# Optimization experiments

Measured on AMD Instinct MI355X. Metric: run time of the kernel, lower is better.

## Reference

```python
import jax, jax.numpy as jnp
import numpy as np

N_NODES = 100000
N_EDGES = 1600000
D_FEAT = 128
ALPHA = 0.1
K_STEPS = 10


def setup_inputs() -> dict:
    key = jax.random.key(0)
    k1, k2, k3 = jax.random.split(key, 3)
    x = jax.random.normal(k1, (N_NODES, D_FEAT), dtype=jnp.float32)
    edge_index = jax.random.randint(k2, (2, N_EDGES), 0, N_NODES, dtype=jnp.int64)
    edge_vals = jax.random.uniform(k3, (N_EDGES,), dtype=jnp.float32)
    return {"x": x, "edge_index": edge_index, "edge_vals": edge_vals}


def _spmm(edge_index, edge_vals, h, n_nodes):
    # out[i] = sum_j A[i, j] * h[j]; row = edge_index[0], col = edge_index[1]
    row, col = edge_index[0], edge_index[1]
    msgs = edge_vals[:, None] * h[col]  # [E, d]
    return jax.ops.segment_sum(msgs, row, num_segments=n_nodes)


def reference(x, edge_index, edge_vals):
    # APPNP propagation: h <- (1 - alpha) * A @ h + alpha * x, K steps.
    # dropout=0.0 -> dropout is the identity (as in the torch module default).
    def body(_, h):
        return (1.0 - ALPHA) * _spmm(edge_index, edge_vals, h, N_NODES) + ALPHA * x

    return jax.lax.fori_loop(0, K_STEPS, body, x)
```

## Files before the change

kernel.cpp:

```cpp
#include <hip/hip_runtime.h>


#define N_NODES 100000
#define N_EDGES 1600000
#define D_FEAT  128
#define ALPHA   0.1f
#define K_STEPS 10
#define MAXDEG  64

#define NBUCK 196
#define BCAP  16000
#define EPB_A 2048

#define SCAN_ELEMS 512
#define SCAN_NBLK  ((N_NODES + SCAN_ELEMS - 1) / SCAN_ELEMS)

static __device__ __forceinline__ float bf2f(unsigned u16) {
    return __uint_as_float(u16 << 16);
}
static __device__ __forceinline__ unsigned f2bf(float f) {
    unsigned u = __float_as_uint(f);
    return (u + 0x7fffu + ((u >> 16) & 1u)) >> 16;
}


__global__ __launch_bounds__(256) void bucket_scatter(const int* __restrict__ rows,
                                                      const int* __restrict__ cols,
                                                      const float* __restrict__ w,
                                                      int* __restrict__ gcount,
                                                      int4* __restrict__ gbuf) {
    __shared__ int h_cnt[NBUCK];
    __shared__ int h_base[NBUCK];
    __shared__ int h_cur[NBUCK];
    const int tid = threadIdx.x;
    for (int i = tid; i < NBUCK; i += 256) { h_cnt[i] = 0; h_cur[i] = 0; }
    __syncthreads();

    const int base_e = blockIdx.x * EPB_A + tid;
    int er[8]; int ec[8]; float ew[8];
    #pragma unroll
    for (int k = 0; k < 8; ++k) {
        int e = base_e + k * 256;
        bool v = (e < N_EDGES);
        er[k] = v ? rows[e] : -1;
        ec[k] = v ? cols[e] : 0;
        ew[k] = v ? w[e] : 0.f;
        if (v) atomicAdd(&h_cnt[er[k] >> 9], 1);
    }
    __syncthreads();
    for (int i = tid; i < NBUCK; i += 256) {
        h_base[i] = (h_cnt[i] > 0) ? atomicAdd(&gcount[i], h_cnt[i]) : 0;
    }
    __syncthreads();
    #pragma unroll
    for (int k = 0; k < 8; ++k) {
        if (er[k] >= 0) {
            int b = er[k] >> 9;
            int p = h_base[b] + atomicAdd(&h_cur[b], 1);
            if (p < BCAP) {
                int4 ent;
                ent.x = er[k];
                ent.y = ec[k];
                ent.z = __float_as_int((1.0f - ALPHA) * ew[k]);
                ent.w = 0;
                gbuf[(size_t)b * BCAP + p] = ent;
            }
        }
    }
}

__global__ __launch_bounds__(256) void bucket_to_csr(const int* __restrict__ gcount,
                                                     const int4* __restrict__ gbuf,
                                                     int* __restrict__ cnt,
                                                     int2* __restrict__ csrp) {
    __shared__ int rcur[512];
    const int tid = threadIdx.x;
    const int b = blockIdx.x;
    for (int i = tid; i < 512; i += 256) rcur[i] = 0;
    __syncthreads();
    int n = gcount[b];
    if (n > BCAP) n = BCAP;
    for (int i = tid; i < n; i += 256) {
        int4 e = gbuf[(size_t)b * BCAP + i];
        int p = atomicAdd(&rcur[e.x & 511], 1);
        if (p < MAXDEG) {
            int2 cw;
            cw.x = e.y;
            cw.y = e.z;
            csrp[((size_t)e.x << 6) + p] = cw;
        }
    }
    __syncthreads();
    const int rowbase = b << 9;
    for (int i = tid; i < 512; i += 256) {
        int row = rowbase + i;
        if (row < N_NODES) cnt[row] = rcur[i];
    }
}


__global__ __launch_bounds__(256) void hist_kernel(const int* __restrict__ rows,
                                                   int* __restrict__ deg) {
    int e = blockIdx.x * 256 + threadIdx.x;
    if (e < N_EDGES) atomicAdd(&deg[rows[e]], 1);
}

__global__ __launch_bounds__(256) void scan_partial(const int* __restrict__ deg,
                                                    int* __restrict__ partial) {
    __shared__ int s[256];
    int b = blockIdx.x, t = threadIdx.x;
    int i0 = b * SCAN_ELEMS + t * 2;
    int v0 = (i0 < N_NODES) ? deg[i0] : 0;
    int v1 = (i0 + 1 < N_NODES) ? deg[i0 + 1] : 0;
    s[t] = v0 + v1;
    __syncthreads();
    for (int off = 128; off > 0; off >>= 1) {
        if (t < off) s[t] += s[t + off];
        __syncthreads();
    }
    if (t == 0) partial[b] = s[0];
}

__global__ __launch_bounds__(256) void scan_top(int* __restrict__ partial) {
    __shared__ int s[256];
    int t = threadIdx.x;
    s[t] = (t < SCAN_NBLK) ? partial[t] : 0;
    __syncthreads();
    for (int off = 1; off < 256; off <<= 1) {
        int v = (t >= off) ? s[t - off] : 0;
        __syncthreads();
        s[t] += v;
        __syncthreads();
    }
    if (t < SCAN_NBLK) partial[t] = (t == 0) ? 0 : s[t - 1];
}

__global__ __launch_bounds__(256) void scan_final(int* __restrict__ deg_cursor,
                                                  const int* __restrict__ partial,
                                                  int* __restrict__ row_ptr) {
    __shared__ int s[256];
    int b = blockIdx.x, t = threadIdx.x;
    int i0 = b * SCAN_ELEMS + t * 2;
    int v0 = (i0 < N_NODES) ? deg_cursor[i0] : 0;
    int v1 = (i0 + 1 < N_NODES) ? deg_cursor[i0 + 1] : 0;
    int pair = v0 + v1;
    s[t] = pair;
    __syncthreads();
    for (int off = 1; off < 256; off <<= 1) {
        int v = (t >= off) ? s[t - off] : 0;
        __syncthreads();
        s[t] += v;
        __syncthreads();
    }
    int ex = partial[b] + s[t] - pair;
    if (i0 < N_NODES)     { row_ptr[i0] = ex;          deg_cursor[i0] = ex; }
    if (i0 + 1 < N_NODES) { row_ptr[i0 + 1] = ex + v0; deg_cursor[i0 + 1] = ex + v0; }
    if (b == 0 && t == 0) row_ptr[N_NODES] = N_EDGES;
}

__global__ __launch_bounds__(256) void scatter_kernel(const int* __restrict__ rows,
                                                      const int* __restrict__ cols,
                                                      const float* __restrict__ w,
                                                      int* __restrict__ cursor,
                                                      int2* __restrict__ csr) {
    int e = blockIdx.x * 256 + threadIdx.x;
    if (e < N_EDGES) {
        int pos = atomicAdd(&cursor[rows[e]], 1);
        int2 cw;
        cw.x = cols[e];
        cw.y = __float_as_int((1.0f - ALPHA) * w[e]);
        csr[pos] = cw;
    }
}

__global__ __launch_bounds__(256) void x_to_bf16(const float2* __restrict__ x2,
                                                 unsigned* __restrict__ xb, int n) {
    int i = blockIdx.x * 256 + threadIdx.x;
    if (i < n) {
        float2 v = x2[i];
        xb[i] = f2bf(v.x) | (f2bf(v.y) << 16);
    }
}


template <bool SRC_BF, bool DST_BF, bool X_BF, bool PAD>
__global__ __launch_bounds__(256) void row_spmm_t(const int* __restrict__ rp,
                                                  const int2* __restrict__ csr,
                                                  const void* __restrict__ xsrc,
                                                  const void* __restrict__ src,
                                                  void* __restrict__ dst) {
    int row = (blockIdx.x * 256 + threadIdx.x) >> 6;
    int lane = threadIdx.x & 63;
    if (row >= N_NODES) return;
    int beg, end;
    if (PAD) {
        int cn = rp[row];
        cn = (cn < MAXDEG) ? cn : MAXDEG;
        beg = row << 6;
        end = beg + cn;
    } else {
        beg = rp[row];
        end = rp[row + 1];
    }

    float xtx, xty;
    if (X_BF) {
        unsigned u = ((const unsigned*)xsrc)[(size_t)row * 64 + lane];
        xtx = ALPHA * bf2f(u & 0xffffu);
        xty = ALPHA * bf2f(u >> 16);
    } else {
        float2 xv = ((const float2*)xsrc)[(size_t)row * 64 + lane];
        xtx = ALPHA * xv.x;
        xty = ALPHA * xv.y;
    }

    const float2*   sf = (const float2*)src;
    const unsigned* sb = (const unsigned*)src;

    float ax[4] = {0.f, 0.f, 0.f, 0.f};
    float ay[4] = {0.f, 0.f, 0.f, 0.f};

    auto gather = [&](int col) -> float2 {
        if (SRC_BF) {
            unsigned u = sb[(size_t)col * 64 + lane];
            float2 v;
            v.x = bf2f(u & 0xffffu);
            v.y = bf2f(u >> 16);
            return v;
        } else {
            return sf[(size_t)col * 64 + lane];
        }
    };

    int j = beg;
    while (j + 16 <= end) {
        int2 cw[16];
        #pragma unroll
        for (int u = 0; u < 16; ++u) cw[u] = csr[j + u];
        float2 v[16];
        #pragma unroll
        for (int u = 0; u < 16; ++u) v[u] = gather(cw[u].x);
        #pragma unroll
        for (int u = 0; u < 16; ++u) {
            float wv = __int_as_float(cw[u].y);
            ax[u & 3] += wv * v[u].x;
            ay[u & 3] += wv * v[u].y;
        }
        j += 16;
    }
    while (j + 8 <= end) {
        int2 cw[8];
        #pragma unroll
        for (int u = 0; u < 8; ++u) cw[u] = csr[j + u];
        float2 v[8];
        #pragma unroll
        for (int u = 0; u < 8; ++u) v[u] = gather(cw[u].x);
        #pragma unroll
        for (int u = 0; u < 8; ++u) {
            float wv = __int_as_float(cw[u].y);
            ax[u & 3] += wv * v[u].x;
            ay[u & 3] += wv * v[u].y;
        }
        j += 8;
    }
    while (j + 4 <= end) {
        int2 cw[4];
        #pragma unroll
        for (int u = 0; u < 4; ++u) cw[u] = csr[j + u];
        float2 v[4];
        #pragma unroll
        for (int u = 0; u < 4; ++u) v[u] = gather(cw[u].x);
        #pragma unroll
        for (int u = 0; u < 4; ++u) {
            float wv = __int_as_float(cw[u].y);
            ax[u] += wv * v[u].x;
            ay[u] += wv * v[u].y;
        }
        j += 4;
    }
    for (; j < end; ++j) {
        int2 cw = csr[j];
        float2 v = gather(cw.x);
        float wv = __int_as_float(cw.y);
        ax[0] += wv * v.x;
        ay[0] += wv * v.y;
    }

    float ox = xtx + (ax[0] + ax[1]) + (ax[2] + ax[3]);
    float oy = xty + (ay[0] + ay[1]) + (ay[2] + ay[3]);

    if (DST_BF) {
        ((unsigned*)dst)[(size_t)row * 64 + lane] = f2bf(ox) | (f2bf(oy) << 16);
    } else {
        float2 o; o.x = ox; o.y = oy;
        ((float2*)dst)[(size_t)row * 64 + lane] = o;
    }
}


__global__ __launch_bounds__(256) void init_step(const float4* __restrict__ x,
                                                 float4* __restrict__ dst, int n4) {
    int i = blockIdx.x * 256 + threadIdx.x;
    if (i < n4) {
        float4 v = x[i];
        dst[i] = make_float4(ALPHA * v.x, ALPHA * v.y, ALPHA * v.z, ALPHA * v.w);
    }
}

__global__ __launch_bounds__(256) void edge_scatter(const int* __restrict__ rows,
                                                    const int* __restrict__ cols,
                                                    const float* __restrict__ w,
                                                    const float* __restrict__ h,
                                                    float* __restrict__ dst) {
    unsigned t = blockIdx.x * 256u + threadIdx.x;
    unsigned e = t >> 5;
    unsigned l = t & 31u;
    if (e >= N_EDGES) return;
    int r = rows[e];
    int c = cols[e];
    float we = (1.0f - ALPHA) * w[e];
    const float4* hc = (const float4*)(h + (size_t)c * D_FEAT);
    float4 v = hc[l];
    float* dr = dst + (size_t)r * D_FEAT + (size_t)l * 4;
    unsafeAtomicAdd(dr + 0, we * v.x);
    unsafeAtomicAdd(dr + 1, we * v.y);
    unsafeAtomicAdd(dr + 2, we * v.z);
    unsafeAtomicAdd(dr + 3, we * v.w);
}

extern "C" void kernel_launch(void* const* d_in, const int* in_sizes, int n_in,
                              void* d_out, int out_size, void* d_ws, size_t ws_size,
                              hipStream_t stream) {
    const float* x  = (const float*)d_in[0];
    const int*   ei = (const int*)d_in[1];
    const float* ev = (const float*)d_in[2];
    const int* rows = ei;
    const int* cols = ei + N_EDGES;
    float* out = (float*)d_out;

    auto align512 = [](size_t o) { return (o + 511) & ~(size_t)511; };

    size_t p_off = 0;
    size_t p_ha   = p_off; p_off = align512(p_off + (size_t)N_NODES * D_FEAT * 2);
    size_t p_hb   = p_off; p_off = align512(p_off + (size_t)N_NODES * D_FEAT * 2);
    size_t p_xb   = p_off; p_off = align512(p_off + (size_t)N_NODES * D_FEAT * 2);
    size_t p_cnt  = p_off; p_off = align512(p_off + (size_t)N_NODES * 4 + NBUCK * 4);
    size_t p_csr  = p_off; p_off = align512(p_off + (size_t)N_NODES * MAXDEG * 8);
    size_t need_pad = p_off;
    static_assert((size_t)NBUCK * BCAP * 16 <= 2 * (size_t)N_NODES * D_FEAT * 2,
                  "gbuf must fit in hb+xb");

    size_t c_off = 0;
    size_t c_ha      = c_off; c_off = align512(c_off + (size_t)N_NODES * D_FEAT * 2);
    size_t c_hb      = c_off; c_off = align512(c_off + (size_t)N_NODES * D_FEAT * 2);
    size_t c_rowptr  = c_off; c_off = align512(c_off + (size_t)(N_NODES + 1) * 4);
    size_t c_cursor  = c_off; c_off = align512(c_off + (size_t)N_NODES * 4);
    size_t c_partial = c_off; c_off = align512(c_off + (size_t)SCAN_NBLK * 4);
    size_t c_csr     = c_off; c_off = align512(c_off + (size_t)N_EDGES * 8);
    size_t need_base = c_off;
    size_t c_xb      = c_off; c_off = align512(c_off + (size_t)N_NODES * D_FEAT * 2);
    size_t need_xb   = c_off;

    const int row_blocks = (N_NODES * 64 + 255) / 256;
    const float2* x2 = (const float2*)x;

    if (ws_size >= need_pad) {
        char* ws = (char*)d_ws;
        void*     h_a    = (void*)(ws + p_ha);
        void*     h_b    = (void*)(ws + p_hb);
        unsigned* xb     = (unsigned*)(ws + p_xb);
        int*      cnt    = (int*)(ws + p_cnt);
        int*      gcount = cnt + N_NODES;
        int2*     csrp   = (int2*)(ws + p_csr);
        int4*     gbuf   = (int4*)(ws + p_hb);

        hipMemsetAsync(cnt, 0, (size_t)N_NODES * 4 + NBUCK * 4, stream);
        const int blocks_a = (N_EDGES + EPB_A - 1) / EPB_A;
        bucket_scatter<<<blocks_a, 256, 0, stream>>>(rows, cols, ev, gcount, gbuf);
        bucket_to_csr<<<NBUCK, 256, 0, stream>>>(gcount, gbuf, cnt, csrp);

        const int nxb = N_NODES * D_FEAT / 2;
        x_to_bf16<<<(nxb + 255) / 256, 256, 0, stream>>>(x2, xb, nxb);

        row_spmm_t<true, true, true, true><<<row_blocks, 256, 0, stream>>>(
            cnt, csrp, (const void*)xb, (const void*)xb, h_a);
        for (int k = 1; k <= 8; ++k) {
            const void* src = (k & 1) ? h_a : h_b;
            void* dst = (k & 1) ? h_b : h_a;
            row_spmm_t<true, true, true, true><<<row_blocks, 256, 0, stream>>>(
                cnt, csrp, (const void*)xb, src, dst);
        }
        row_spmm_t<true, false, false, true><<<row_blocks, 256, 0, stream>>>(
            cnt, csrp, (const void*)x2, (const void*)h_a, (void*)out);
    } else if (ws_size >= need_base) {
        char* ws = (char*)d_ws;
        void*  h_a     = (void*)(ws + c_ha);
        void*  h_b     = (void*)(ws + c_hb);
        int*   row_ptr = (int*)(ws + c_rowptr);
        int*   cursor  = (int*)(ws + c_cursor);
        int*   partial = (int*)(ws + c_partial);
        int2*  csr     = (int2*)(ws + c_csr);
        unsigned* xb   = (unsigned*)(ws + c_xb);
        const bool has_xb = (ws_size >= need_xb);
        const int edge_blocks_1t = (N_EDGES + 255) / 256;

        hipMemsetAsync(cursor, 0, (size_t)N_NODES * 4, stream);
        hist_kernel<<<edge_blocks_1t, 256, 0, stream>>>(rows, cursor);
        scan_partial<<<SCAN_NBLK, 256, 0, stream>>>(cursor, partial);
        scan_top<<<1, 256, 0, stream>>>(partial);
        scan_final<<<SCAN_NBLK, 256, 0, stream>>>(cursor, partial, row_ptr);
        scatter_kernel<<<edge_blocks_1t, 256, 0, stream>>>(rows, cols, ev, cursor, csr);

        if (has_xb) {
            const int nxb = N_NODES * D_FEAT / 2;
            x_to_bf16<<<(nxb + 255) / 256, 256, 0, stream>>>(x2, xb, nxb);
            row_spmm_t<true, true, true, false><<<row_blocks, 256, 0, stream>>>(
                row_ptr, csr, (const void*)xb, (const void*)xb, h_a);
            for (int k = 1; k <= 8; ++k) {
                const void* src = (k & 1) ? h_a : h_b;
                void* dst = (k & 1) ? h_b : h_a;
                row_spmm_t<true, true, true, false><<<row_blocks, 256, 0, stream>>>(
                    row_ptr, csr, (const void*)xb, src, dst);
            }
            row_spmm_t<true, false, false, false><<<row_blocks, 256, 0, stream>>>(
                row_ptr, csr, (const void*)x2, (const void*)h_a, (void*)out);
        } else {
            row_spmm_t<false, true, false, false><<<row_blocks, 256, 0, stream>>>(
                row_ptr, csr, (const void*)x2, (const void*)x, h_a);
            for (int k = 1; k <= 8; ++k) {
                const void* src = (k & 1) ? h_a : h_b;
                void* dst = (k & 1) ? h_b : h_a;
                row_spmm_t<true, true, false, false><<<row_blocks, 256, 0, stream>>>(
                    row_ptr, csr, (const void*)x2, src, dst);
            }
            row_spmm_t<true, false, false, false><<<row_blocks, 256, 0, stream>>>(
                row_ptr, csr, (const void*)x2, (const void*)h_a, (void*)out);
        }
    } else {
        float* wsf = (float*)d_ws;
        const int n4 = N_NODES * D_FEAT / 4;
        const int init_blocks = (n4 + 255) / 256;
        const int edge_blocks = (N_EDGES * 32 + 255) / 256;
        for (int k = 0; k < K_STEPS; ++k) {
            const float* src = (k == 0) ? x : ((k & 1) ? wsf : out);
            float* dst = (k & 1) ? out : wsf;
            init_step<<<init_blocks, 256, 0, stream>>>((const float4*)x, (float4*)dst, n4);
            edge_scatter<<<edge_blocks, 256, 0, stream>>>(rows, cols, ev, src, dst);
        }
    }
}
```

Measured before the change: 804.3 us.

## Split each row's wavefront into four edge groups with 16-byte bf16 gathers

Adds a new SpMM kernel in which each 64-lane wavefront handles one row as four 16-lane subgroups. Each subgroup processes different edges and gathers a full 256-byte bf16 feature row with uint4 loads, and the partial sums are combined with cross-lane shuffles. This replaces narrow 4-byte-per-lane gathers and serial per-edge iteration with wider loads and more edges in flight, aiming for better memory-level parallelism on a gather-bound kernel. The CSR buffer is padded by 512 bytes so the out-of-range index reads stay in bounds. The 16-edge unroll in the old kernel, now used only on the fallback path, is removed.

```diff
diff --git a/kernel.cpp b/kernel.cpp
--- a/kernel.cpp
+++ b/kernel.cpp
@@ -179,6 +179,110 @@
     if (i < n) {
         float2 v = x2[i];
         xb[i] = f2bf(v.x) | (f2bf(v.y) << 16);
+    }
+}
+
+
+template <bool DST_BF, bool X_BF>
+__global__ __launch_bounds__(256) void row_spmm_q(const int* __restrict__ rp,
+                                                  const int2* __restrict__ csr,
+                                                  const void* __restrict__ xsrc,
+                                                  const unsigned* __restrict__ src,
+                                                  void* __restrict__ dst) {
+    int row = (blockIdx.x * 256 + threadIdx.x) >> 6;
+    int lane = threadIdx.x & 63;
+    if (row >= N_NODES) return;
+    int cn = rp[row];
+    cn = (cn < MAXDEG) ? cn : MAXDEG;
+    const int beg = row << 6;
+    const int end = beg + cn;
+    const int sub = lane >> 4;
+    const int fl  = lane & 15;
+
+    uint4 xu; float4 xa, xc;
+    if (X_BF) {
+        xu = ((const uint4*)xsrc)[(size_t)row * 16 + fl];
+    } else {
+        xa = ((const float4*)xsrc)[(size_t)row * 32 + 2 * fl];
+        xc = ((const float4*)xsrc)[(size_t)row * 32 + 2 * fl + 1];
+    }
+
+    const uint4* s4 = (const uint4*)src;
+
+    float acc[8];
+    #pragma unroll
+    for (int k = 0; k < 8; ++k) acc[k] = 0.f;
+
+    for (int j = beg; j < end; j += 8) {
+        int i0 = j + sub;
+        int i1 = j + 4 + sub;
+        bool v0 = i0 < end;
+        bool v1 = i1 < end;
+        int2 c0 = csr[i0];
+        int2 c1 = csr[i1];
+        int col0 = v0 ? c0.x : 0;
+        int col1 = v1 ? c1.x : 0;
+        float w0 = v0 ? __int_as_float(c0.y) : 0.f;
+        float w1 = v1 ? __int_as_float(c1.y) : 0.f;
+        uint4 g0 = s4[(size_t)col0 * 16 + fl];
+        uint4 g1 = s4[(size_t)col1 * 16 + fl];
+        acc[0] += w0 * bf2f(g0.x & 0xffffu);
+        acc[1] += w0 * bf2f(g0.x >> 16);
+        acc[2] += w0 * bf2f(g0.y & 0xffffu);
+        acc[3] += w0 * bf2f(g0.y >> 16);
+        acc[4] += w0 * bf2f(g0.z & 0xffffu);
+        acc[5] += w0 * bf2f(g0.z >> 16);
+        acc[6] += w0 * bf2f(g0.w & 0xffffu);
+        acc[7] += w0 * bf2f(g0.w >> 16);
+        acc[0] += w1 * bf2f(g1.x & 0xffffu);
+        acc[1] += w1 * bf2f(g1.x >> 16);
+        acc[2] += w1 * bf2f(g1.y & 0xffffu);
+        acc[3] += w1 * bf2f(g1.y >> 16);
+        acc[4] += w1 * bf2f(g1.z & 0xffffu);
+        acc[5] += w1 * bf2f(g1.z >> 16);
+        acc[6] += w1 * bf2f(g1.w & 0xffffu);
+        acc[7] += w1 * bf2f(g1.w >> 16);
+    }
+
+    #pragma unroll
+    for (int k = 0; k < 8; ++k) {
+        acc[k] += __shfl_xor(acc[k], 16);
+        acc[k] += __shfl_xor(acc[k], 32);
+    }
+
+    if (X_BF) {
+        acc[0] += ALPHA * bf2f(xu.x & 0xffffu);
+        acc[1] += ALPHA * bf2f(xu.x >> 16);
+        acc[2] += ALPHA * bf2f(xu.y & 0xffffu);
+        acc[3] += ALPHA * bf2f(xu.y >> 16);
+        acc[4] += ALPHA * bf2f(xu.z & 0xffffu);
+        acc[5] += ALPHA * bf2f(xu.z >> 16);
+        acc[6] += ALPHA * bf2f(xu.w & 0xffffu);
+        acc[7] += ALPHA * bf2f(xu.w >> 16);
+    } else {
+        acc[0] += ALPHA * xa.x; acc[1] += ALPHA * xa.y;
+        acc[2] += ALPHA * xa.z; acc[3] += ALPHA * xa.w;
+        acc[4] += ALPHA * xc.x; acc[5] += ALPHA * xc.y;
+        acc[6] += ALPHA * xc.z; acc[7] += ALPHA * xc.w;
+    }
+
+    if (DST_BF) {
+        if (sub == 0) {
+            uint4 o;
+            o.x = f2bf(acc[0]) | (f2bf(acc[1]) << 16);
+            o.y = f2bf(acc[2]) | (f2bf(acc[3]) << 16);
+            o.z = f2bf(acc[4]) | (f2bf(acc[5]) << 16);
+            o.w = f2bf(acc[6]) | (f2bf(acc[7]) << 16);
+            ((uint4*)dst)[(size_t)row * 16 + fl] = o;
+        }
+    } else {
+        if (sub == 0) {
+            float4 o; o.x = acc[0]; o.y = acc[1]; o.z = acc[2]; o.w = acc[3];
+            ((float4*)dst)[(size_t)row * 32 + 2 * fl] = o;
+        } else if (sub == 1) {
+            float4 o; o.x = acc[4]; o.y = acc[5]; o.z = acc[6]; o.w = acc[7];
+            ((float4*)dst)[(size_t)row * 32 + 2 * fl + 1] = o;
+        }
     }
 }
 
@@ -233,21 +337,6 @@
     };
 
     int j = beg;
-    while (j + 16 <= end) {
-        int2 cw[16];
-        #pragma unroll
-        for (int u = 0; u < 16; ++u) cw[u] = csr[j + u];
-        float2 v[16];
-        #pragma unroll
-        for (int u = 0; u < 16; ++u) v[u] = gather(cw[u].x);
-        #pragma unroll
-        for (int u = 0; u < 16; ++u) {
-            float wv = __int_as_float(cw[u].y);
-            ax[u & 3] += wv * v[u].x;
-            ay[u & 3] += wv * v[u].y;
-        }
-        j += 16;
-    }
     while (j + 8 <= end) {
         int2 cw[8];
         #pragma unroll
@@ -345,7 +434,7 @@
     size_t p_hb   = p_off; p_off = align512(p_off + (size_t)N_NODES * D_FEAT * 2);
     size_t p_xb   = p_off; p_off = align512(p_off + (size_t)N_NODES * D_FEAT * 2);
     size_t p_cnt  = p_off; p_off = align512(p_off + (size_t)N_NODES * 4 + NBUCK * 4);
-    size_t p_csr  = p_off; p_off = align512(p_off + (size_t)N_NODES * MAXDEG * 8);
+    size_t p_csr  = p_off; p_off = align512(p_off + (size_t)N_NODES * MAXDEG * 8 + 512);
     size_t need_pad = p_off;
     static_assert((size_t)NBUCK * BCAP * 16 <= 2 * (size_t)N_NODES * D_FEAT * 2,
                   "gbuf must fit in hb+xb");
@@ -382,16 +471,16 @@
         const int nxb = N_NODES * D_FEAT / 2;
         x_to_bf16<<<(nxb + 255) / 256, 256, 0, stream>>>(x2, xb, nxb);
 
-        row_spmm_t<true, true, true, true><<<row_blocks, 256, 0, stream>>>(
-            cnt, csrp, (const void*)xb, (const void*)xb, h_a);
+        row_spmm_q<true, true><<<row_blocks, 256, 0, stream>>>(
+            cnt, csrp, (const void*)xb, xb, h_a);
         for (int k = 1; k <= 8; ++k) {
             const void* src = (k & 1) ? h_a : h_b;
             void* dst = (k & 1) ? h_b : h_a;
-            row_spmm_t<true, true, true, true><<<row_blocks, 256, 0, stream>>>(
-                cnt, csrp, (const void*)xb, src, dst);
-        }
-        row_spmm_t<true, false, false, true><<<row_blocks, 256, 0, stream>>>(
-            cnt, csrp, (const void*)x2, (const void*)h_a, (void*)out);
+            row_spmm_q<true, true><<<row_blocks, 256, 0, stream>>>(
+                cnt, csrp, (const void*)xb, (const unsigned*)src, dst);
+        }
+        row_spmm_q<false, false><<<row_blocks, 256, 0, stream>>>(
+            cnt, csrp, (const void*)x2, (const unsigned*)h_a, (void*)out);
     } else if (ws_size >= need_base) {
         char* ws = (char*)d_ws;
         void*  h_a     = (void*)(ws + c_ha);
```

Result: faster. 777.7 us (-3.3%).
